# Kernel tuning notes

Hardware: AMD Instinct MI355X
Metric: run time of the kernel (lower is better)

Reference implementation:

```python
import jax, jax.numpy as jnp
import numpy as np

N, DIN, DOUT, E, K = 65536, 256, 256, 8, 2

def setup_inputs() -> dict:
    key = jax.random.key(0)
    k1, k2, k3, k4 = jax.random.split(key, 4)
    x = jax.random.normal(k1, (N, DIN), dtype=jnp.float32)
    Wr = jax.random.normal(k2, (DIN, E), dtype=jnp.float32) * (DIN ** -0.5)   # router Linear (no bias)
    We = jax.random.normal(k3, (E, DIN, DOUT), dtype=jnp.float32) * (DIN ** -0.5)  # expert Linear weights
    be = jax.random.normal(k4, (E, DOUT), dtype=jnp.float32) * 0.01               # expert Linear biases
    return {"x": x, "Wr": Wr, "We": We, "be": be}

def reference(x, Wr, We, be):
    # router: softmax over experts (eval mode -> no noise)
    probs = jax.nn.softmax(x @ Wr, axis=1)                    # [N, E]
    w, sel = jax.lax.top_k(probs, K)                          # [N, K]
    w = w / jnp.sum(w, axis=1, keepdims=True)                 # renormalize top-k weights
    # dense combine weights: scatter top-k weights back to [N, E]
    combine = jnp.zeros_like(probs).at[jnp.arange(x.shape[0])[:, None], sel].add(w)
    # all-expert outputs, then weighted combine (same math as gather/matmul/index_add loop)
    y_all = jnp.einsum('ni,eio->neo', x, We) + be[None, :, :]  # [N, E, DOUT]
    out = jnp.einsum('neo,ne->no', y_all, combine)             # [N, DOUT]
    return out
```

## Files before the change

kernel.cpp:

```cpp
#include <hip/hip_runtime.h>

#define N_TOK 65536
#define DIN   256
#define DOUT  256
#define NEXP  8
#define NPAIR 28

typedef __bf16 bf16x8 __attribute__((ext_vector_type(8)));
typedef __bf16 bf16x4 __attribute__((ext_vector_type(4)));
typedef float  f32x4  __attribute__((ext_vector_type(4)));

__device__ __forceinline__ void cp16_g2l(const void* g, void* l) {
  auto gp = (const __attribute__((address_space(1))) unsigned int*)(unsigned long long)g;
  auto lp = (__attribute__((address_space(3))) unsigned int*)(unsigned long long)l;
  __builtin_amdgcn_global_load_lds(gp, lp, 16, 0, 0);
}

__global__ __launch_bounds__(256) void prep_kernel(const float* __restrict__ We,
                                                   __bf16* __restrict__ Wt,
                                                   int* __restrict__ cnt) {
  __shared__ float T[64 * 65];
  int bid = blockIdx.x;
  if (bid == 0 && threadIdx.x < NPAIR) cnt[threadIdx.x] = 0;
  int e = bid >> 4;
  int tk = (bid >> 2) & 3, tn = bid & 3;
  int k0 = tk * 64, n0 = tn * 64;
  int tid = threadIdx.x;
  int cr = tid >> 6;
  int cc = tid & 63;
#pragma unroll
  for (int i = 0; i < 16; i++) {
    int k = i * 4 + cr;
    T[cc * 65 + k] = We[(size_t)(e * 256 + k0 + k) * 256 + n0 + cc];
  }
  __syncthreads();
#pragma unroll
  for (int i = 0; i < 16; i++) {
    int n = i * 4 + cr;
    Wt[(size_t)(e * 256 + n0 + n) * 256 + k0 + cc] = (__bf16)T[n * 65 + cc];
  }
}

__global__ __launch_bounds__(64) void router_kernel(const float* __restrict__ x,
                                                    const float* __restrict__ Wr,
                                                    __bf16* __restrict__ xb,
                                                    int* __restrict__ cnt,
                                                    unsigned short* __restrict__ pidx,
                                                    float* __restrict__ pw) {
  __shared__ float X[64 * 32];
  __shared__ int lcnt[NPAIR];
  __shared__ int gbase[NPAIR];
  int tid = threadIdx.x;
  if (tid < NPAIR) lcnt[tid] = 0;

  int tokBase = blockIdx.x * 64;
  int token = tokBase + tid;

  const int sr = tid >> 3;
  const int so = tid & 7;
  const int po = so ^ sr;
  const int ro = tid & 7;

  float acc[NEXP];
#pragma unroll
  for (int e = 0; e < NEXP; e++) acc[e] = 0.f;

  float4 v[8];
#pragma unroll
  for (int i = 0; i < 8; i++)
    v[i] = *(const float4*)&x[(size_t)(tokBase + i * 8 + sr) * DIN + so * 4];

  for (int kc = 0; kc < 8; kc++) {
#pragma unroll
    for (int i = 0; i < 8; i++) {
      int r = i * 8 + sr;
      *(float4*)&X[((r * 8 + po)) * 4] = v[i];
      bf16x4 bv;
      bv[0] = (__bf16)v[i].x; bv[1] = (__bf16)v[i].y;
      bv[2] = (__bf16)v[i].z; bv[3] = (__bf16)v[i].w;
      *(bf16x4*)&xb[(size_t)(tokBase + r) * DIN + kc * 32 + so * 4] = bv;
    }
    __syncthreads();
    if (kc < 7) {
#pragma unroll
      for (int i = 0; i < 8; i++)
        v[i] = *(const float4*)&x[(size_t)(tokBase + i * 8 + sr) * DIN + (kc + 1) * 32 + so * 4];
    }
#pragma unroll
    for (int i4 = 0; i4 < 8; i4++) {
      float4 xv = *(const float4*)&X[((tid * 8 + (i4 ^ ro))) * 4];
      const float* w0 = &Wr[(kc * 32 + i4 * 4) * NEXP];
#pragma unroll
      for (int e = 0; e < NEXP; e++)
        acc[e] += xv.x * w0[e] + xv.y * w0[NEXP + e] + xv.z * w0[2 * NEXP + e] + xv.w * w0[3 * NEXP + e];
    }
    __syncthreads();
  }

  int best = 0;
#pragma unroll
  for (int e = 1; e < NEXP; e++) if (acc[e] > acc[best]) best = e;
  int sec = (best == 0) ? 1 : 0;
#pragma unroll
  for (int e = 0; e < NEXP; e++)
    if (e != best && e != sec && acc[e] > acc[sec]) sec = e;
  float l3 = -1e30f;
#pragma unroll
  for (int e = 0; e < NEXP; e++)
    if (e != best && e != sec) l3 = fmaxf(l3, acc[e]);

  float diff = acc[sec] - acc[best];
  bool need = (acc[sec] - l3) < 5e-3f;
  if (__any(need)) {
    if (need) {
      const float4* xr = (const float4*)(x + (size_t)token * DIN);
      double d[NEXP];
#pragma unroll
      for (int e = 0; e < NEXP; e++) d[e] = 0.0;
      for (int i4 = 0; i4 < DIN / 4; i4++) {
        float4 vv = xr[i4];
        const float* w0 = &Wr[(i4 * 4) * NEXP];
#pragma unroll
        for (int e = 0; e < NEXP; e++)
          d[e] += (double)vv.x * w0[e] + (double)vv.y * w0[NEXP + e] +
                  (double)vv.z * w0[2 * NEXP + e] + (double)vv.w * w0[3 * NEXP + e];
      }
      best = 0;
#pragma unroll
      for (int e = 1; e < NEXP; e++) if (d[e] > d[best]) best = e;
      sec = (best == 0) ? 1 : 0;
#pragma unroll
      for (int e = 0; e < NEXP; e++)
        if (e != best && e != sec && d[e] > d[sec]) sec = e;
      diff = (float)(d[sec] - d[best]);
    }
  }

  float wb = 1.f / (1.f + expf(diff));
  int a, b2; float wa;
  if (best < sec) { a = best; b2 = sec; wa = wb; }
  else            { a = sec;  b2 = best; wa = 1.f - wb; }
  int p = a * (15 - a) / 2 + (b2 - a - 1);

  int lpos = atomicAdd(&lcnt[p], 1);
  __syncthreads();
  if (tid < NPAIR) gbase[tid] = atomicAdd(&cnt[tid], lcnt[tid]);
  __syncthreads();
  int pos = gbase[p] + lpos;
  pidx[p * N_TOK + pos] = (unsigned short)token;
  pw[p * N_TOK + pos] = wa;
}

__global__ __launch_bounds__(256) void moe_gemm_kernel(const __bf16* __restrict__ xb,
                                                       const __bf16* __restrict__ Wt,
                                                       const float* __restrict__ be,
                                                       const int* __restrict__ cnt,
                                                       const unsigned short* __restrict__ pidx,
                                                       const float* __restrict__ pw,
                                                       float* __restrict__ out) {
  __shared__ __bf16 As[128 * 64];
  __shared__ unsigned short tokL[128];
  __shared__ float wL[128];
  __shared__ int meta[4];

  int tid = threadIdx.x;
  int tile = blockIdx.x >> 2;
  int nh = blockIdx.x & 3;

  if (tid == 0) {
    int s = 0, pp = -1, lt = 0, c = 0;
    for (int q = 0; q < NPAIR; q++) {
      int cq = cnt[q];
      int tq = (cq + 127) >> 7;
      if (tile < s + tq) { pp = q; lt = tile - s; c = cq; break; }
      s += tq;
    }
    meta[0] = pp; meta[1] = lt; meta[2] = c;
  }
  __syncthreads();
  int p = meta[0];
  if (p < 0) return;
  int lt = meta[1], cnt_p = meta[2];

  int a = 0, rem = p;
  while (rem >= 7 - a) { rem -= 7 - a; a++; }
  int b2 = a + 1 + rem;
  int r0 = lt * 128;

  if (tid < 128) {
    int gr = r0 + tid;
    tokL[tid] = (gr < cnt_p) ? pidx[p * N_TOK + gr] : (unsigned short)0;
    wL[tid]   = (gr < cnt_p) ? pw[p * N_TOK + gr] : 0.f;
  }
  __syncthreads();

  const int lane = tid & 63, wid = tid >> 6;
  const int wm = wid & 1, wn = wid >> 1;
  const int c16 = lane & 15, quad = lane >> 4;

  const int r_base = tid >> 3;
  const int s8 = (tid & 7) ^ (r_base & 7);
  size_t grow[4];
#pragma unroll
  for (int i = 0; i < 4; i++)
    grow[i] = (size_t)tokL[r_base + 32 * i] * DIN + s8 * 8;

  const __bf16* WtA = Wt + ((size_t)a * DOUT + nh * 64) * DIN;
  const __bf16* WtB = Wt + ((size_t)b2 * DOUT + nh * 64) * DIN;

  f32x4 accA[4][2], accB[4][2];
#pragma unroll
  for (int mi = 0; mi < 4; mi++)
#pragma unroll
    for (int ni = 0; ni < 2; ni++)
#pragma unroll
      for (int r = 0; r < 4; r++) { accA[mi][ni][r] = 0.f; accB[mi][ni][r] = 0.f; }

  for (int kc = 0; kc < 4; kc++) {
#pragma unroll
    for (int i = 0; i < 4; i++) {
      int slot = tid + 256 * i;
      cp16_g2l(xb + grow[i] + kc * 64, &As[slot * 8]);
    }
    __builtin_amdgcn_s_waitcnt(0x0F70);
    __syncthreads();
#pragma unroll
    for (int ks = 0; ks < 2; ks++) {
      bf16x8 af[4], ba[2], bb[2];
#pragma unroll
      for (int mi = 0; mi < 4; mi++) {
        int row = wm * 64 + mi * 16 + c16;
        int oct = ks * 4 + quad;
        af[mi] = *(const bf16x8*)&As[(row * 8 + (oct ^ (row & 7))) * 8];
      }
#pragma unroll
      for (int ni = 0; ni < 2; ni++) {
        int col = wn * 32 + ni * 16 + c16;
        int koff = kc * 64 + ks * 32 + quad * 8;
        ba[ni] = *(const bf16x8*)&WtA[(size_t)col * DIN + koff];
        bb[ni] = *(const bf16x8*)&WtB[(size_t)col * DIN + koff];
      }
#pragma unroll
      for (int mi = 0; mi < 4; mi++)
#pragma unroll
        for (int ni = 0; ni < 2; ni++) {
          accA[mi][ni] = __builtin_amdgcn_mfma_f32_16x16x32_bf16(af[mi], ba[ni], accA[mi][ni], 0, 0, 0);
          accB[mi][ni] = __builtin_amdgcn_mfma_f32_16x16x32_bf16(af[mi], bb[ni], accB[mi][ni], 0, 0, 0);
        }
    }
    __syncthreads();
  }

#pragma unroll
  for (int ni = 0; ni < 2; ni++) {
    int gcol = nh * 64 + wn * 32 + ni * 16 + c16;
    float bea = be[a * DOUT + gcol];
    float beb = be[b2 * DOUT + gcol];
#pragma unroll
    for (int mi = 0; mi < 4; mi++) {
#pragma unroll
      for (int r = 0; r < 4; r++) {
        int row = wm * 64 + mi * 16 + quad * 4 + r;
        if (r0 + row < cnt_p) {
          float w = wL[row];
          out[(size_t)tokL[row] * DOUT + gcol] =
              w * (accA[mi][ni][r] + bea) + (1.f - w) * (accB[mi][ni][r] + beb);
        }
      }
    }
  }
}

extern "C" void kernel_launch(void* const* d_in, const int* in_sizes, int n_in,
                              void* d_out, int out_size, void* d_ws, size_t ws_size,
                              hipStream_t stream) {
  const float* x  = (const float*)d_in[0];
  const float* Wr = (const float*)d_in[1];
  const float* We = (const float*)d_in[2];
  const float* be = (const float*)d_in[3];
  float* out = (float*)d_out;

  char* w = (char*)d_ws;
  __bf16* Wt = (__bf16*)w;
  __bf16* xb = (__bf16*)(w + (1u << 20));
  int* cnt = (int*)(w + (33u << 20));
  unsigned short* pidx = (unsigned short*)(w + (33u << 20) + 512);
  float* pw = (float*)(w + (33u << 20) + 512 + (size_t)NPAIR * N_TOK * 2);

  prep_kernel<<<128, 256, 0, stream>>>(We, Wt, cnt);
  router_kernel<<<N_TOK / 64, 64, 0, stream>>>(x, Wr, xb, cnt, pidx, pw);
  moe_gemm_kernel<<<540 * 4, 256, 0, stream>>>(xb, Wt, be, cnt, pidx, pw, out);
}
```

Measured before the change: 235.4 us.

## Split router logit reduction across four waves per 64-token block

The router kernel goes from 64 to 256 threads per block. Each of four waves handles a quarter of each 64-wide K chunk, and the partial logits are summed through a shared-memory buffer. This is meant to raise memory-level parallelism and occupancy in the bandwidth-bound pass that reads x and writes the bf16 copy. After the reduction only the first wave continues to top-k selection and scattering, so the barriers around the per-pair atomics are removed. The changed summation order alters float rounding of the logits, and the removed barriers rely on that remaining work staying within one wavefront.

Measured after the change: 212.7 us. 1.11x faster.

```diff
diff --git a/kernel.cpp b/kernel.cpp
--- a/kernel.cpp
+++ b/kernel.cpp
@@ -41,55 +41,57 @@
   }
 }
 
-__global__ __launch_bounds__(64) void router_kernel(const float* __restrict__ x,
-                                                    const float* __restrict__ Wr,
-                                                    __bf16* __restrict__ xb,
-                                                    int* __restrict__ cnt,
-                                                    unsigned short* __restrict__ pidx,
-                                                    float* __restrict__ pw) {
-  __shared__ float X[64 * 32];
+__global__ __launch_bounds__(256) void router_kernel(const float* __restrict__ x,
+                                                     const float* __restrict__ Wr,
+                                                     __bf16* __restrict__ xb,
+                                                     int* __restrict__ cnt,
+                                                     unsigned short* __restrict__ pidx,
+                                                     float* __restrict__ pw) {
+  __shared__ float X[64 * 64];
+  __shared__ float P[64 * 36];
   __shared__ int lcnt[NPAIR];
   __shared__ int gbase[NPAIR];
   int tid = threadIdx.x;
   if (tid < NPAIR) lcnt[tid] = 0;
 
+  const int w = __builtin_amdgcn_readfirstlane(tid >> 6);
+  const int t = tid & 63;
   int tokBase = blockIdx.x * 64;
-  int token = tokBase + tid;
-
-  const int sr = tid >> 3;
-  const int so = tid & 7;
-  const int po = so ^ sr;
-  const int ro = tid & 7;
+
+  const int srow = tid >> 4;
+  const int so16 = tid & 15;
+  const int spo  = so16 ^ (srow & 7);
 
   float acc[NEXP];
 #pragma unroll
   for (int e = 0; e < NEXP; e++) acc[e] = 0.f;
 
-  float4 v[8];
-#pragma unroll
-  for (int i = 0; i < 8; i++)
-    v[i] = *(const float4*)&x[(size_t)(tokBase + i * 8 + sr) * DIN + so * 4];
-
-  for (int kc = 0; kc < 8; kc++) {
-#pragma unroll
-    for (int i = 0; i < 8; i++) {
-      int r = i * 8 + sr;
-      *(float4*)&X[((r * 8 + po)) * 4] = v[i];
+  float4 v[4];
+#pragma unroll
+  for (int i = 0; i < 4; i++)
+    v[i] = *(const float4*)&x[(size_t)(tokBase + srow + 16 * i) * DIN + so16 * 4];
+
+  for (int c = 0; c < 4; c++) {
+#pragma unroll
+    for (int i = 0; i < 4; i++) {
+      int r = srow + 16 * i;
+      *(float4*)&X[r * 64 + spo * 4] = v[i];
       bf16x4 bv;
       bv[0] = (__bf16)v[i].x; bv[1] = (__bf16)v[i].y;
       bv[2] = (__bf16)v[i].z; bv[3] = (__bf16)v[i].w;
-      *(bf16x4*)&xb[(size_t)(tokBase + r) * DIN + kc * 32 + so * 4] = bv;
+      *(bf16x4*)&xb[(size_t)(tokBase + r) * DIN + c * 64 + so16 * 4] = bv;
     }
     __syncthreads();
-    if (kc < 7) {
-#pragma unroll
-      for (int i = 0; i < 8; i++)
-        v[i] = *(const float4*)&x[(size_t)(tokBase + i * 8 + sr) * DIN + (kc + 1) * 32 + so * 4];
-    }
-#pragma unroll
-    for (int i4 = 0; i4 < 8; i4++) {
-      float4 xv = *(const float4*)&X[((tid * 8 + (i4 ^ ro))) * 4];
-      const float* w0 = &Wr[(kc * 32 + i4 * 4) * NEXP];
+    if (c < 3) {
+#pragma unroll
+      for (int i = 0; i < 4; i++)
+        v[i] = *(const float4*)&x[(size_t)(tokBase + srow + 16 * i) * DIN + (c + 1) * 64 + so16 * 4];
+    }
+#pragma unroll
+    for (int i4 = 0; i4 < 4; i4++) {
+      int po = (w * 4 + i4) ^ (t & 7);
+      float4 xv = *(const float4*)&X[t * 64 + po * 4];
+      const float* w0 = &Wr[(c * 64 + w * 16 + i4 * 4) * NEXP];
 #pragma unroll
       for (int e = 0; e < NEXP; e++)
         acc[e] += xv.x * w0[e] + xv.y * w0[NEXP + e] + xv.z * w0[2 * NEXP + e] + xv.w * w0[3 * NEXP + e];
@@ -97,20 +99,44 @@
     __syncthreads();
   }
 
+  f32x4 lo, hi;
+#pragma unroll
+  for (int e = 0; e < 4; e++) { lo[e] = acc[e]; hi[e] = acc[4 + e]; }
+  *(f32x4*)&P[t * 36 + w * 8]     = lo;
+  *(f32x4*)&P[t * 36 + w * 8 + 4] = hi;
+  __syncthreads();
+  if (tid >= 64) return;
+
+  int token = tokBase + tid;
+
+  f32x4 pa0 = *(const f32x4*)&P[tid * 36 + 0];
+  f32x4 pa1 = *(const f32x4*)&P[tid * 36 + 8];
+  f32x4 pa2 = *(const f32x4*)&P[tid * 36 + 16];
+  f32x4 pa3 = *(const f32x4*)&P[tid * 36 + 24];
+  f32x4 pb0 = *(const f32x4*)&P[tid * 36 + 4];
+  f32x4 pb1 = *(const f32x4*)&P[tid * 36 + 12];
+  f32x4 pb2 = *(const f32x4*)&P[tid * 36 + 20];
+  f32x4 pb3 = *(const f32x4*)&P[tid * 36 + 28];
+  f32x4 sA = ((pa0 + pa1) + pa2) + pa3;
+  f32x4 sB = ((pb0 + pb1) + pb2) + pb3;
+  float lg[NEXP];
+#pragma unroll
+  for (int e = 0; e < 4; e++) { lg[e] = sA[e]; lg[4 + e] = sB[e]; }
+
   int best = 0;
 #pragma unroll
-  for (int e = 1; e < NEXP; e++) if (acc[e] > acc[best]) best = e;
+  for (int e = 1; e < NEXP; e++) if (lg[e] > lg[best]) best = e;
   int sec = (best == 0) ? 1 : 0;
 #pragma unroll
   for (int e = 0; e < NEXP; e++)
-    if (e != best && e != sec && acc[e] > acc[sec]) sec = e;
+    if (e != best && e != sec && lg[e] > lg[sec]) sec = e;
   float l3 = -1e30f;
 #pragma unroll
   for (int e = 0; e < NEXP; e++)
-    if (e != best && e != sec) l3 = fmaxf(l3, acc[e]);
-
-  float diff = acc[sec] - acc[best];
-  bool need = (acc[sec] - l3) < 5e-3f;
+    if (e != best && e != sec) l3 = fmaxf(l3, lg[e]);
+
+  float diff = lg[sec] - lg[best];
+  bool need = (lg[sec] - l3) < 5e-3f;
   if (__any(need)) {
     if (need) {
       const float4* xr = (const float4*)(x + (size_t)token * DIN);
@@ -143,9 +169,7 @@
   int p = a * (15 - a) / 2 + (b2 - a - 1);
 
   int lpos = atomicAdd(&lcnt[p], 1);
-  __syncthreads();
   if (tid < NPAIR) gbase[tid] = atomicAdd(&cnt[tid], lcnt[tid]);
-  __syncthreads();
   int pos = gbase[p] + lpos;
   pidx[p * N_TOK + pos] = (unsigned short)token;
   pw[p * N_TOK + pos] = wa;
@@ -288,6 +312,6 @@
   float* pw = (float*)(w + (33u << 20) + 512 + (size_t)NPAIR * N_TOK * 2);
 
   prep_kernel<<<128, 256, 0, stream>>>(We, Wt, cnt);
-  router_kernel<<<N_TOK / 64, 64, 0, stream>>>(x, Wr, xb, cnt, pidx, pw);
+  router_kernel<<<N_TOK / 64, 256, 0, stream>>>(x, Wr, xb, cnt, pidx, pw);
   moe_gemm_kernel<<<540 * 4, 256, 0, stream>>>(xb, Wt, be, cnt, pidx, pw, out);
 }
```
